# Kernel tuning notes

Hardware: AMD Instinct MI355X
Metric: run time of the kernel (lower is better)

Reference implementation:

```python
import jax, jax.numpy as jnp
import numpy as np

ROUTER_TEMP = 1.0
SCALING = 16.0 / 8.0  # lora_alpha / r


def setup_inputs() -> dict:
    key = jax.random.key(0)
    ks = jax.random.split(key, 6)
    B, S, D, O, E, R = 4, 2048, 4096, 4096, 8, 8
    return {
        "x": jax.random.normal(ks[0], (B, S, D), dtype=jnp.float32),
        "W_base": jax.random.normal(ks[1], (O, D), dtype=jnp.float32) * 0.02,
        "b_base": jax.random.normal(ks[2], (O,), dtype=jnp.float32) * 0.02,
        "lora_A": jax.random.normal(ks[3], (E, R, D), dtype=jnp.float32) * 0.02,
        "lora_B": jax.random.normal(ks[4], (E, O, R), dtype=jnp.float32) * 0.02,
        "router_W": jax.random.normal(ks[5], (E, D), dtype=jnp.float32) * 0.02,
        "router_b": jnp.zeros((E,), dtype=jnp.float32),
    }


def reference(x, W_base, b_base, lora_A, lora_B, router_W, router_b):
    # Base linear: [B,S,D] @ [D,O] + b -> [B,S,O]
    result = jnp.einsum("bsd,od->bso", x, W_base) + b_base

    # Router over mean-pooled sequence: [B,D] -> [B,E]
    x_router = x.mean(axis=1)
    logits = jnp.einsum("bd,ed->be", x_router, router_W) + router_b
    weights = jax.nn.softmax(logits / ROUTER_TEMP, axis=-1)  # [B,E]

    # Per-expert LoRA: down-project to small r, weight by router, up-project.
    h = jnp.einsum("bsd,erd->bser", x, lora_A)            # [B,S,E,r] (small)
    hw = h * weights[:, None, :, None]                      # router-weighted
    lora_out = jnp.einsum("bser,eor->bso", hw, lora_B)     # [B,S,O]

    return result + lora_out * SCALING
```

## Files before the change

### kernel.cpp

```cpp
#include <hip/hip_runtime.h>
#include <hip/hip_bf16.h>


typedef unsigned short u16;
typedef __attribute__((ext_vector_type(8))) short short8;
typedef __attribute__((ext_vector_type(8))) unsigned short u16x8;
typedef __attribute__((ext_vector_type(4))) float f32x4;

#define AS1(p) ((const __attribute__((address_space(1))) void*)(p))
#define AS3(p) ((__attribute__((address_space(3))) void*)(p))

constexpr int KM   = 4160;
constexpr int NOUT = 4096;

__device__ __forceinline__ u16 f2bf(float f) {
    union { float f; unsigned int u; } v; v.f = f;
    unsigned int r = v.u + 0x7fffu + ((v.u >> 16) & 1u);
    return (u16)(r >> 16);
}

__global__ __launch_bounds__(256) void k_convx(const float* __restrict__ x,
                                               u16* __restrict__ Xext,
                                               float* __restrict__ colpart) {
    const int t = threadIdx.x;
    const int row0 = (blockIdx.x >> 7) * 2048 + (blockIdx.x & 127) * 16;
    float4 cs[4] = {{0,0,0,0},{0,0,0,0},{0,0,0,0},{0,0,0,0}};
    for (int r = 0; r < 16; ++r) {
        size_t roff = (size_t)(row0 + r) * 4096;
        #pragma unroll
        for (int g = 0; g < 2; ++g) {
            int col = g * 2048 + t * 8;
            const float4* p = (const float4*)(x + roff + col);
            float4 v0 = p[0], v1 = p[1];
            cs[2*g].x += v0.x; cs[2*g].y += v0.y; cs[2*g].z += v0.z; cs[2*g].w += v0.w;
            cs[2*g+1].x += v1.x; cs[2*g+1].y += v1.y; cs[2*g+1].z += v1.z; cs[2*g+1].w += v1.w;
            u16x8 o;
            o[0]=f2bf(v0.x); o[1]=f2bf(v0.y); o[2]=f2bf(v0.z); o[3]=f2bf(v0.w);
            o[4]=f2bf(v1.x); o[5]=f2bf(v1.y); o[6]=f2bf(v1.z); o[7]=f2bf(v1.w);
            *(u16x8*)(Xext + (size_t)(row0 + r) * KM + col) = o;
        }
    }
    float* cp = colpart + (size_t)blockIdx.x * 4096;
    #pragma unroll
    for (int g = 0; g < 2; ++g) {
        *(float4*)(cp + g * 2048 + t * 8)     = cs[2*g];
        *(float4*)(cp + g * 2048 + t * 8 + 4) = cs[2*g+1];
    }
}

__global__ __launch_bounds__(256) void k_logit(const float* __restrict__ colpart,
                                               const float* __restrict__ rW,
                                               float* __restrict__ logits) {
    const int b = blockIdx.x >> 3, e = blockIdx.x & 7;
    const int t = threadIdx.x;
    const int c0 = t * 16;
    float4 rw[4];
    #pragma unroll
    for (int j = 0; j < 4; ++j) rw[j] = *(const float4*)(rW + e * 4096 + c0 + j * 4);
    float acc = 0.f;
    for (int sc = 0; sc < 128; ++sc) {
        const float4* p = (const float4*)(colpart + ((size_t)(b * 128 + sc)) * 4096 + c0);
        #pragma unroll
        for (int j = 0; j < 4; ++j) {
            float4 v = p[j];
            acc += v.x * rw[j].x + v.y * rw[j].y + v.z * rw[j].z + v.w * rw[j].w;
        }
    }
    __shared__ float red[256];
    red[t] = acc;
    __syncthreads();
    for (int off = 128; off > 0; off >>= 1) {
        if (t < off) red[t] += red[t + off];
        __syncthreads();
    }
    if (t == 0) logits[b * 8 + e] = red[0];
}

__global__ void k_conv8(const float* __restrict__ src, u16* __restrict__ dst) {
    size_t t = (size_t)blockIdx.x * 256 + threadIdx.x;
    size_t base = t * 8;
    size_t row = base >> 12;
    int col = (int)(base & 4095);
    const float4* s = (const float4*)(src + base);
    float4 v0 = s[0], v1 = s[1];
    u16x8 o;
    o[0]=f2bf(v0.x); o[1]=f2bf(v0.y); o[2]=f2bf(v0.z); o[3]=f2bf(v0.w);
    o[4]=f2bf(v1.x); o[5]=f2bf(v1.y); o[6]=f2bf(v1.z); o[7]=f2bf(v1.w);
    *(u16x8*)(dst + row * KM + col) = o;
}

__global__ void k_wlora(const float* __restrict__ lb, u16* __restrict__ Wext) {
    int f = blockIdx.x * 256 + threadIdx.x;
    int e = f >> 15, o = (f >> 3) & 4095, r = f & 7;
    Wext[(size_t)o * KM + 4096 + e * 8 + r] = f2bf(lb[f]);
}

__global__ void k_abf(const float* __restrict__ la, u16* __restrict__ Abf) {
    int f = blockIdx.x * 256 + threadIdx.x;
    Abf[f] = f2bf(la[f]);
}

__global__ __launch_bounds__(256) void k_hgemm(const u16* __restrict__ Xb,
                                               const u16* __restrict__ Ab,
                                               const float* __restrict__ logits,
                                               const float* __restrict__ rb,
                                               u16* __restrict__ Hout) {
    __shared__ u16 As[8 * 1024];
    __shared__ u16 Bs[8 * 2048];
    __shared__ float Red[4 * 2048];
    __shared__ float wscL[8];
    const int tid = threadIdx.x, lane = tid & 63, w = tid >> 6;
    const int m0 = blockIdx.x * 32;
    const int b = blockIdx.x >> 6;

    if (tid < 8) {
        float l[8], mx = -1e30f;
        #pragma unroll
        for (int j = 0; j < 8; ++j) {
            l[j] = logits[b * 8 + j] * (1.0f / 2048.0f) + rb[j];
            mx = fmaxf(mx, l[j]);
        }
        float s = 0.f;
        #pragma unroll
        for (int j = 0; j < 8; ++j) s += expf(l[j] - mx);
        wscL[tid] = 2.0f * expf(l[tid] - mx) / s;
    }
    asm volatile("s_waitcnt vmcnt(0)" ::: "memory");

    f32x4 acc[2][4] = {};
    const int kbase = w * 1024;

    auto issue = [&](int it, int buf) {
        const int kt = kbase + it * 32;
        u16* Aw = As + (w * 2 + buf) * 1024;
        u16* Bw = Bs + (w * 2 + buf) * 2048;
        #pragma unroll
        for (int i = 0; i < 2; ++i) {
            int f = lane + i * 64;
            __builtin_amdgcn_global_load_lds(
                AS1(Xb + (size_t)(m0 + (f >> 2)) * KM + kt + (f & 3) * 8),
                AS3(Aw + f * 8), 16, 0, 0);
        }
        #pragma unroll
        for (int i = 0; i < 4; ++i) {
            int f = lane + i * 64;
            __builtin_amdgcn_global_load_lds(
                AS1(Ab + (size_t)(f >> 2) * 4096 + kt + (f & 3) * 8),
                AS3(Bw + f * 8), 16, 0, 0);
        }
    };

    issue(0, 0);
    for (int it = 0; it < 32; ++it) {
        const int buf = it & 1;
        if (it + 1 < 32) {
            issue(it + 1, buf ^ 1);
            asm volatile("s_waitcnt vmcnt(6)" ::: "memory");
        } else {
            asm volatile("s_waitcnt vmcnt(0)" ::: "memory");
        }
        const u16* Aw = As + (w * 2 + buf) * 1024;
        const u16* Bw = Bs + (w * 2 + buf) * 2048;
        short8 af[2], bfr[4];
        #pragma unroll
        for (int mi = 0; mi < 2; ++mi)
            af[mi] = *(const short8*)(Aw + (mi * 16 + (lane & 15)) * 32 + (lane >> 4) * 8);
        #pragma unroll
        for (int nj = 0; nj < 4; ++nj)
            bfr[nj] = *(const short8*)(Bw + (nj * 16 + (lane & 15)) * 32 + (lane >> 4) * 8);
        #pragma unroll
        for (int mi = 0; mi < 2; ++mi)
            #pragma unroll
            for (int nj = 0; nj < 4; ++nj)
                acc[mi][nj] = __builtin_amdgcn_mfma_f32_16x16x32_bf16(af[mi], bfr[nj], acc[mi][nj], 0, 0, 0);
        asm volatile("" ::: "memory");
    }

    const int quad = lane >> 4, lcol = lane & 15;
    #pragma unroll
    for (int mi = 0; mi < 2; ++mi)
        #pragma unroll
        for (int nj = 0; nj < 4; ++nj)
            #pragma unroll
            for (int r = 0; r < 4; ++r)
                Red[w * 2048 + (mi * 16 + quad * 4 + r) * 64 + nj * 16 + lcol] = acc[mi][nj][r];
    __syncthreads();

    const int o = tid * 8, row = o >> 6, col = o & 63;
    float s0=0,s1=0,s2=0,s3=0,s4=0,s5=0,s6=0,s7=0;
    #pragma unroll
    for (int ww = 0; ww < 4; ++ww) {
        const float4* p = (const float4*)(Red + ww * 2048 + o);
        float4 v0 = p[0], v1 = p[1];
        s0+=v0.x; s1+=v0.y; s2+=v0.z; s3+=v0.w;
        s4+=v1.x; s5+=v1.y; s6+=v1.z; s7+=v1.w;
    }
    const float wgt = wscL[col >> 3];
    u16x8 out;
    out[0]=f2bf(s0*wgt); out[1]=f2bf(s1*wgt); out[2]=f2bf(s2*wgt); out[3]=f2bf(s3*wgt);
    out[4]=f2bf(s4*wgt); out[5]=f2bf(s5*wgt); out[6]=f2bf(s6*wgt); out[7]=f2bf(s7*wgt);
    *(u16x8*)(Hout + (size_t)(m0 + row) * KM + 4096 + col) = out;
}

__global__ __launch_bounds__(256) void k_main(const u16* __restrict__ A, const u16* __restrict__ B,
                                              const float* __restrict__ bias, float* __restrict__ C) {
    __shared__ u16 As[128 * 32];
    __shared__ u16 Bs[128 * 32];
    const int tid = threadIdx.x;
    const int lane = tid & 63;
    const int wave = tid >> 6;
    const int wm = (wave >> 1) * 64;
    const int wn = (wave & 1) * 64;
    const int m0 = blockIdx.y * 128;
    const int n0 = blockIdx.x * 128;

    f32x4 acc[4][4] = {};

    const int arow0 = tid >> 2, ak = (tid & 3) * 8;
    const int arow1 = (tid + 256) >> 2;
    const u16* Ag0 = A + (size_t)(m0 + arow0) * KM + ak;
    const u16* Ag1 = A + (size_t)(m0 + arow1) * KM + ak;
    const u16* Bg0 = B + (size_t)(n0 + arow0) * KM + ak;
    const u16* Bg1 = B + (size_t)(n0 + arow1) * KM + ak;
    u16* Asp0 = As + tid * 8;
    u16* Asp1 = As + (tid + 256) * 8;
    u16* Bsp0 = Bs + tid * 8;
    u16* Bsp1 = Bs + (tid + 256) * 8;

    const int aoff = (wm + (lane & 15)) * 32 + (lane >> 4) * 8;
    const int boff = (wn + (lane & 15)) * 32 + (lane >> 4) * 8;

    for (int kt = 0; kt < KM; kt += 32) {
        __builtin_amdgcn_global_load_lds(AS1(Ag0 + kt), AS3(Asp0), 16, 0, 0);
        __builtin_amdgcn_global_load_lds(AS1(Ag1 + kt), AS3(Asp1), 16, 0, 0);
        __builtin_amdgcn_global_load_lds(AS1(Bg0 + kt), AS3(Bsp0), 16, 0, 0);
        __builtin_amdgcn_global_load_lds(AS1(Bg1 + kt), AS3(Bsp1), 16, 0, 0);
        __syncthreads();
        short8 af[4], bf[4];
        #pragma unroll
        for (int i = 0; i < 4; i++) af[i] = *(const short8*)(As + aoff + i * 16 * 32);
        #pragma unroll
        for (int j = 0; j < 4; j++) bf[j] = *(const short8*)(Bs + boff + j * 16 * 32);
        #pragma unroll
        for (int i = 0; i < 4; i++)
            #pragma unroll
            for (int j = 0; j < 4; j++)
                acc[i][j] = __builtin_amdgcn_mfma_f32_16x16x32_bf16(af[i], bf[j], acc[i][j], 0, 0, 0);
        __syncthreads();
    }

    const int lrow = (lane >> 4) * 4, lcol = lane & 15;
    #pragma unroll
    for (int j = 0; j < 4; j++) {
        int col = n0 + wn + j * 16 + lcol;
        float bv = bias[col];
        #pragma unroll
        for (int i = 0; i < 4; i++) {
            int row = m0 + wm + i * 16 + lrow;
            float* Cp = C + (size_t)row * NOUT + col;
            #pragma unroll
            for (int r = 0; r < 4; r++)
                Cp[(size_t)r * NOUT] = acc[i][j][r] + bv;
        }
    }
}

extern "C" void kernel_launch(void* const* d_in, const int* in_sizes, int n_in,
                              void* d_out, int out_size, void* d_ws, size_t ws_size,
                              hipStream_t stream) {
    const float* x  = (const float*)d_in[0];
    const float* Wb = (const float*)d_in[1];
    const float* bb = (const float*)d_in[2];
    const float* lA = (const float*)d_in[3];
    const float* lB = (const float*)d_in[4];
    const float* rW = (const float*)d_in[5];
    const float* rb = (const float*)d_in[6];
    float* out = (float*)d_out;

    char* ws = (char*)d_ws;
    float* logits = (float*)ws;
    u16* Abf      = (u16*)(ws + 256);
    u16* Xext     = (u16*)(ws + (1 << 20));
    u16* Wext     = (u16*)(ws + (1 << 20) + 68157440ULL);
    float* colpart = (float*)Wext;

    k_abf   <<<1024, 256, 0, stream>>>(lA, Abf);
    k_convx <<<512,  256, 0, stream>>>(x, Xext, colpart);
    k_logit <<<32,   256, 0, stream>>>(colpart, rW, logits);
    k_hgemm <<<256,  256, 0, stream>>>(Xext, Abf, logits, rb, Xext);
    k_conv8 <<<8192, 256, 0, stream>>>(Wb, Wext);
    k_wlora <<<1024, 256, 0, stream>>>(lB, Wext);
    k_main  <<<dim3(32, 64), 256, 0, stream>>>(Xext, Wext, bb, out);
}
```

Baseline: 643.6 us.

## Rewrite main GEMM with 256x256 tiles, double-buffered swizzled LDS and interleaved phases

Replaces the 128x128 single-buffered bf16 MFMA GEMM with a 512-thread 256x256 tile kernel. It uses 128-wide K steps, XOR-swizzled LDS to avoid bank conflicts, double buffering with global_load_lds prefetch overlapped with MFMA phases, setprio and sched barriers, and a grouped block-index swizzle for L2 reuse. K is padded from 4160 to 4224 with zero columns in both operands so it divides into 128-wide tiles, and the workspace offsets are adjusted to match. The 128 KB LDS per block limits occupancy, and the extra zero padding adds a little work.

New measurement: 564.1 us. -12.3%, faster.

```diff
diff --git a/kernel.cpp b/kernel.cpp
--- a/kernel.cpp
+++ b/kernel.cpp
@@ -10,7 +10,7 @@
 #define AS1(p) ((const __attribute__((address_space(1))) void*)(p))
 #define AS3(p) ((__attribute__((address_space(3))) void*)(p))
 
-constexpr int KM   = 4160;
+constexpr int KM   = 4224;
 constexpr int NOUT = 4096;
 
 __device__ __forceinline__ u16 f2bf(float f) {
@@ -93,6 +93,7 @@
     int f = blockIdx.x * 256 + threadIdx.x;
     int e = f >> 15, o = (f >> 3) & 4095, r = f & 7;
     Wext[(size_t)o * KM + 4096 + e * 8 + r] = f2bf(lb[f]);
+    Wext[(size_t)(f >> 6) * KM + 4160 + (f & 63)] = 0;
 }
 
 __global__ void k_abf(const float* __restrict__ la, u16* __restrict__ Abf) {
@@ -200,67 +201,144 @@
     out[0]=f2bf(s0*wgt); out[1]=f2bf(s1*wgt); out[2]=f2bf(s2*wgt); out[3]=f2bf(s3*wgt);
     out[4]=f2bf(s4*wgt); out[5]=f2bf(s5*wgt); out[6]=f2bf(s6*wgt); out[7]=f2bf(s7*wgt);
     *(u16x8*)(Hout + (size_t)(m0 + row) * KM + 4096 + col) = out;
-}
-
-__global__ __launch_bounds__(256) void k_main(const u16* __restrict__ A, const u16* __restrict__ B,
-                                              const float* __restrict__ bias, float* __restrict__ C) {
-    __shared__ u16 As[128 * 32];
-    __shared__ u16 Bs[128 * 32];
+    u16x8 zz = {0,0,0,0,0,0,0,0};
+    *(u16x8*)(Hout + (size_t)(m0 + (tid >> 3)) * KM + 4160 + (tid & 7) * 8) = zz;
+}
+
+
+#define LDB_(bufB) do { \
+    const char* bp_ = ldsc + bBaseB + (bufB); \
+    _Pragma("unroll") \
+    for (int nj_ = 0; nj_ < 4; ++nj_) { \
+        bf[nj_][0] = *(const short8*)(bp_ + nj_ * 2048 + rdk0); \
+        bf[nj_][1] = *(const short8*)(bp_ + nj_ * 2048 + rdk1); \
+    } \
+} while (0)
+
+#define LDA_(bufB, pq) do { \
+    const char* ap_ = ldsc + aBaseB + (bufB) + (pq) * 4096; \
+    af[0][0] = *(const short8*)(ap_ + rdk0); \
+    af[0][1] = *(const short8*)(ap_ + rdk1); \
+    af[1][0] = *(const short8*)(ap_ + 2048 + rdk0); \
+    af[1][1] = *(const short8*)(ap_ + 2048 + rdk1); \
+} while (0)
+
+#define MFMA_(pq) do { \
+    __builtin_amdgcn_s_barrier(); \
+    asm volatile("s_waitcnt lgkmcnt(0)" ::: "memory"); \
+    __builtin_amdgcn_sched_barrier(0); \
+    __builtin_amdgcn_s_setprio(1); \
+    _Pragma("unroll") \
+    for (int q_ = 0; q_ < 2; ++q_) { \
+        _Pragma("unroll") \
+        for (int nj_ = 0; nj_ < 4; ++nj_) { \
+            acc[(pq)*2+q_][nj_] = __builtin_amdgcn_mfma_f32_16x16x32_bf16(af[q_][0], bf[nj_][0], acc[(pq)*2+q_][nj_], 0, 0, 0); \
+            acc[(pq)*2+q_][nj_] = __builtin_amdgcn_mfma_f32_16x16x32_bf16(af[q_][1], bf[nj_][1], acc[(pq)*2+q_][nj_], 0, 0, 0); \
+        } \
+    } \
+    __builtin_amdgcn_s_setprio(0); \
+    __builtin_amdgcn_sched_barrier(0); \
+} while (0)
+
+#define ENDPH_() __builtin_amdgcn_s_barrier()
+
+__global__ __launch_bounds__(512, 2) void k_main(const u16* __restrict__ A, const u16* __restrict__ B,
+                                                 const float* __restrict__ bias, float* __restrict__ C) {
+    __shared__ __align__(16) u16 lds[65536];
+    const char* ldsc = (const char*)lds;
     const int tid = threadIdx.x;
     const int lane = tid & 63;
-    const int wave = tid >> 6;
-    const int wm = (wave >> 1) * 64;
-    const int wn = (wave & 1) * 64;
-    const int m0 = blockIdx.y * 128;
-    const int n0 = blockIdx.x * 128;
-
-    f32x4 acc[4][4] = {};
-
-    const int arow0 = tid >> 2, ak = (tid & 3) * 8;
-    const int arow1 = (tid + 256) >> 2;
-    const u16* Ag0 = A + (size_t)(m0 + arow0) * KM + ak;
-    const u16* Ag1 = A + (size_t)(m0 + arow1) * KM + ak;
-    const u16* Bg0 = B + (size_t)(n0 + arow0) * KM + ak;
-    const u16* Bg1 = B + (size_t)(n0 + arow1) * KM + ak;
-    u16* Asp0 = As + tid * 8;
-    u16* Asp1 = As + (tid + 256) * 8;
-    u16* Bsp0 = Bs + tid * 8;
-    u16* Bsp1 = Bs + (tid + 256) * 8;
-
-    const int aoff = (wm + (lane & 15)) * 32 + (lane >> 4) * 8;
-    const int boff = (wn + (lane & 15)) * 32 + (lane >> 4) * 8;
-
-    for (int kt = 0; kt < KM; kt += 32) {
-        __builtin_amdgcn_global_load_lds(AS1(Ag0 + kt), AS3(Asp0), 16, 0, 0);
-        __builtin_amdgcn_global_load_lds(AS1(Ag1 + kt), AS3(Asp1), 16, 0, 0);
-        __builtin_amdgcn_global_load_lds(AS1(Bg0 + kt), AS3(Bsp0), 16, 0, 0);
-        __builtin_amdgcn_global_load_lds(AS1(Bg1 + kt), AS3(Bsp1), 16, 0, 0);
-        __syncthreads();
-        short8 af[4], bf[4];
-        #pragma unroll
-        for (int i = 0; i < 4; i++) af[i] = *(const short8*)(As + aoff + i * 16 * 32);
-        #pragma unroll
-        for (int j = 0; j < 4; j++) bf[j] = *(const short8*)(Bs + boff + j * 16 * 32);
-        #pragma unroll
-        for (int i = 0; i < 4; i++)
+    const int w = tid >> 6;
+    const int wm = w >> 2;
+    const int wn = w & 3;
+    const int lr = lane & 15, hi = lane >> 4;
+
+    const int bid = blockIdx.x;
+    const int swz = (bid & 7) * 64 + (bid >> 3);
+    const int m0 = (swz >> 4) * 256;
+    const int n0 = (swz & 15) * 256;
+
+    const int csw = (lr & 7) << 4;
+    const int rdk0 = lr * 128 + ((hi * 16) ^ csw);
+    const int rdk1 = lr * 128 + ((64 + hi * 16) ^ csw);
+    const int aBaseB = wm * 16384;
+    const int bBaseB = 32768 + (wn >> 1) * 16384 + (wn & 1) * 8192;
+
+    const int srow = tid >> 3;
+    const int scol = ((tid & 7) ^ ((tid >> 3) & 7)) * 8;
+    const int so0 = srow * KM + scol;
+    const int so1 = (64 + srow) * KM + scol;
+    const u16* Am0 = A + (size_t)m0 * KM;
+    const u16* Am1 = A + (size_t)(m0 + 128) * KM;
+    const u16* Bm0 = B + (size_t)n0 * KM;
+    const u16* Bm1 = B + (size_t)(n0 + 128) * KM;
+    u16* ldst = lds + tid * 8;
+
+    auto stage = [&](const u16* src, int t, int regionEl) {
+        __builtin_amdgcn_global_load_lds(AS1(src + so0 + t * 64), AS3(ldst + regionEl), 16, 0, 0);
+        __builtin_amdgcn_global_load_lds(AS1(src + so1 + t * 64), AS3(ldst + regionEl + 4096), 16, 0, 0);
+    };
+
+    f32x4 acc[8][4] = {};
+
+    stage(Bm0, 0, 16384);
+    stage(Bm1, 0, 24576);
+    stage(Am0, 0, 0);
+    stage(Am1, 0, 8192);
+    stage(Bm0, 1, 32768 + 16384);
+    stage(Bm1, 1, 32768 + 24576);
+    asm volatile("s_waitcnt vmcnt(4)" ::: "memory");
+    __builtin_amdgcn_s_barrier();
+
+    #pragma unroll 1
+    for (int i = 0; i < 33; ++i) {
+        const int t = i * 2;
+        const bool nl = (i < 32);
+        short8 af[2][2];
+        short8 bf[4][2];
+        LDB_(0); LDA_(0, 0);
+        stage(Am0, t + 1, 32768);
+        MFMA_(0); ENDPH_();
+        LDA_(0, 1);
+        stage(Am1, t + 1, 32768 + 8192);
+        MFMA_(1); ENDPH_();
+        LDA_(0, 2);
+        if (nl) stage(Bm0, t + 2, 16384);
+        MFMA_(2); ENDPH_();
+        LDA_(0, 3);
+        if (nl) stage(Bm1, t + 2, 24576);
+        MFMA_(3);
+        if (nl) { asm volatile("s_waitcnt vmcnt(4)" ::: "memory"); }
+        else    { asm volatile("s_waitcnt vmcnt(0)" ::: "memory"); }
+        ENDPH_();
+        LDB_(65536); LDA_(65536, 0);
+        if (nl) stage(Am0, t + 2, 0);
+        MFMA_(0); ENDPH_();
+        LDA_(65536, 1);
+        if (nl) stage(Am1, t + 2, 8192);
+        MFMA_(1); ENDPH_();
+        LDA_(65536, 2);
+        if (nl) stage(Bm0, t + 3, 32768 + 16384);
+        MFMA_(2); ENDPH_();
+        LDA_(65536, 3);
+        if (nl) stage(Bm1, t + 3, 32768 + 24576);
+        MFMA_(3);
+        if (nl) { asm volatile("s_waitcnt vmcnt(4)" ::: "memory"); }
+        ENDPH_();
+    }
+
+    const int colb = n0 + wn * 64 + lr;
+    const int rowb = m0 + wm * 128 + hi * 4;
+    #pragma unroll
+    for (int nj = 0; nj < 4; ++nj) {
+        const int col = colb + nj * 16;
+        const float bv = bias[col];
+        #pragma unroll
+        for (int mi = 0; mi < 8; ++mi) {
+            float* Cp = C + (size_t)(rowb + mi * 16) * NOUT + col;
             #pragma unroll
-            for (int j = 0; j < 4; j++)
-                acc[i][j] = __builtin_amdgcn_mfma_f32_16x16x32_bf16(af[i], bf[j], acc[i][j], 0, 0, 0);
-        __syncthreads();
-    }
-
-    const int lrow = (lane >> 4) * 4, lcol = lane & 15;
-    #pragma unroll
-    for (int j = 0; j < 4; j++) {
-        int col = n0 + wn + j * 16 + lcol;
-        float bv = bias[col];
-        #pragma unroll
-        for (int i = 0; i < 4; i++) {
-            int row = m0 + wm + i * 16 + lrow;
-            float* Cp = C + (size_t)row * NOUT + col;
-            #pragma unroll
-            for (int r = 0; r < 4; r++)
-                Cp[(size_t)r * NOUT] = acc[i][j][r] + bv;
+            for (int r = 0; r < 4; ++r)
+                Cp[(size_t)r * NOUT] = acc[mi][nj][r] + bv;
         }
     }
 }
@@ -280,8 +358,8 @@
     char* ws = (char*)d_ws;
     float* logits = (float*)ws;
     u16* Abf      = (u16*)(ws + 256);
-    u16* Xext     = (u16*)(ws + (1 << 20));
-    u16* Wext     = (u16*)(ws + (1 << 20) + 68157440ULL);
+    u16* Xext     = (u16*)(ws + 524800);
+    u16* Wext     = (u16*)(ws + 524800 + 69206016ULL);
     float* colpart = (float*)Wext;
 
     k_abf   <<<1024, 256, 0, stream>>>(lA, Abf);
@@ -290,5 +368,5 @@
     k_hgemm <<<256,  256, 0, stream>>>(Xext, Abf, logits, rb, Xext);
     k_conv8 <<<8192, 256, 0, stream>>>(Wb, Wext);
     k_wlora <<<1024, 256, 0, stream>>>(lB, Wext);
-    k_main  <<<dim3(32, 64), 256, 0, stream>>>(Xext, Wext, bb, out);
-}
+    k_main  <<<512,  512, 0, stream>>>(Xext, Wext, bb, out);
+}
```
